# Optimization experiments

Hardware: AMD Instinct MI355X
Metric: run time of the kernel (lower is better)

## Reference

```python
import jax, jax.numpy as jnp
import numpy as np
from jax import lax

TAU = 10.0
THR = 1.0
ALPHA = float(np.exp(-1.0 / TAU))  # leak factor exp(-dt/tau), dt=1


def conv2d(x, w, pad):
    # x: [N,C,H,W], w: [O,I,kh,kw]
    return lax.conv_general_dilated(
        x, w, window_strides=(1, 1), padding=[(pad, pad), (pad, pad)],
        dimension_numbers=('NCHW', 'OIHW', 'NCHW'))


def avgpool(x, k):
    n, c, h, w = x.shape
    return x.reshape(n, c, h // k, k, w // k, k).mean(axis=(3, 5))


def exp_leak(x):
    # x: [T, ...]; v[t] = alpha*v[t-1] + x[t]; outputs membrane each step
    def step(v, xt):
        v = ALPHA * v + xt
        return v, v
    _, y = lax.scan(step, jnp.zeros_like(x[0]), x)
    return y


def lif(x):
    # LIF with SingleSpike + MembraneSubtract reset (norm_input=False)
    def step(v, xt):
        v = ALPHA * v + xt
        s = (v >= THR).astype(v.dtype)
        return v - s * THR, s
    _, s = lax.scan(step, jnp.zeros_like(x[0]), x)
    return s


def forward(x, conv1_w, conv2_w, lin_w):
    B, T = x.shape[:2]
    h = avgpool(conv2d(x.reshape(B * T, 2, 32, 32), conv1_w, 2), 4)  # [BT,4,8,8]
    h = h.reshape(B, T, 4, 8, 8).swapaxes(0, 1)                       # [T,B,4,8,8]
    h = lif(exp_leak(h)).swapaxes(0, 1).reshape(B * T, 4, 8, 8)
    h = avgpool(conv2d(h, conv2_w, 1), 2)                             # [BT,8,4,4]
    h = h.reshape(B, T, 8, 4, 4).swapaxes(0, 1)                       # [T,B,8,4,4]
    h = lif(exp_leak(h)).swapaxes(0, 1).reshape(B, T, 8 * 4 * 4)      # [B,T,128]
    return jnp.einsum('btf,of->bto', h, lin_w)                        # [B,T,2]


def setup_inputs() -> dict:
    key = jax.random.key(0)
    k1, k2, k3, k4 = jax.random.split(key, 4)
    B, T = 128, 100
    x = jax.random.uniform(k1, (B, T, 2, 32, 32), dtype=jnp.float32)
    conv1_w = jax.random.normal(k2, (4, 2, 5, 5), dtype=jnp.float32) / np.sqrt(2 * 5 * 5)
    conv2_w = jax.random.normal(k3, (8, 4, 3, 3), dtype=jnp.float32) / np.sqrt(4 * 3 * 3)
    lin_w = jax.random.normal(k4, (2, 128), dtype=jnp.float32) / np.sqrt(128)
    return {'x': x, 'conv1_w': conv1_w, 'conv2_w': conv2_w, 'lin_w': lin_w}


def reference(x, conv1_w, conv2_w, lin_w):
    return forward(x, conv1_w, conv2_w, lin_w)
```

## Files before the change

kernel.cpp:

```cpp
#include <hip/hip_runtime.h>

#define ALPHA 0.90483741803595957f

__global__ void prep_weights(const float* __restrict__ w1, const float* __restrict__ w2,
                             float* __restrict__ w1e, float* __restrict__ w2e) {
    int idx = blockIdx.x * 256 + threadIdx.x;
    if (idx < 512) {
        int v = idx & 7, u = (idx >> 3) & 7, ch = (idx >> 6) & 1, oc = idx >> 7;
        float s = 0.f;
        for (int a = 0; a < 5; ++a) {
            int i = u - a; if (i < 0 || i > 3) continue;
            for (int b = 0; b < 5; ++b) {
                int j = v - b; if (j < 0 || j > 3) continue;
                s += w1[((oc * 2 + ch) * 5 + a) * 5 + b];
            }
        }
        w1e[idx] = s * (1.f / 16.f);
    } else if (idx < 1024) {
        int k = idx - 512;
        int v = k & 3, u = (k >> 2) & 3, ch = (k >> 4) & 3, oc = k >> 6;
        float s = 0.f;
        for (int a = 0; a < 3; ++a) {
            int i = u - a; if (i < 0 || i > 1) continue;
            for (int b = 0; b < 3; ++b) {
                int j = v - b; if (j < 0 || j > 1) continue;
                s += w2[((oc * 4 + ch) * 3 + a) * 3 + b];
            }
        }
        w2e[k] = s * 0.25f;
    }
}

__global__ __launch_bounds__(256) void conv1_pool(const float* __restrict__ x,
                                                  const float* __restrict__ w1e,
                                                  float* __restrict__ y1) {
    __shared__ __align__(16) float tile[4][2][36][36];
    int tid = threadIdx.x;

    float4* t4 = (float4*)&tile[0][0][0][0];
    #pragma unroll
    for (int k = 0; k < 11; ++k) {
        int i = tid + k * 256;
        if (i < 2592) t4[i] = make_float4(0.f, 0.f, 0.f, 0.f);
    }
    __syncthreads();

    int li = tid >> 6, pos = tid & 63;
    long gi = (long)blockIdx.x * 4 + li;
    const float* src = x + gi * 2048;
    #pragma unroll
    for (int k = 0; k < 8; ++k) {
        int e = k * 256 + pos * 4;
        float4 d = *(const float4*)(src + e);
        int ch = e >> 10, rem = e & 1023, r = rem >> 5, c = rem & 31;
        float* dst = &tile[li][ch][r + 2][c + 2];
        dst[0] = d.x; dst[1] = d.y; dst[2] = d.z; dst[3] = d.w;
    }
    __syncthreads();

    int p = pos >> 3, q = pos & 7;
    float acc0 = 0.f, acc1 = 0.f, acc2 = 0.f, acc3 = 0.f;
    #pragma unroll
    for (int ch = 0; ch < 2; ++ch) {
        #pragma unroll
        for (int r = 0; r < 8; ++r) {
            const float* row = &tile[li][ch][4 * p + r][4 * q];
            float4 a = *(const float4*)row;
            float4 b = *(const float4*)(row + 4);
            float in[8] = {a.x, a.y, a.z, a.w, b.x, b.y, b.z, b.w};
            #pragma unroll
            for (int c = 0; c < 8; ++c) {
                float xi = in[c];
                acc0 += w1e[((0 * 2 + ch) * 8 + r) * 8 + c] * xi;
                acc1 += w1e[((1 * 2 + ch) * 8 + r) * 8 + c] * xi;
                acc2 += w1e[((2 * 2 + ch) * 8 + r) * 8 + c] * xi;
                acc3 += w1e[((3 * 2 + ch) * 8 + r) * 8 + c] * xi;
            }
        }
    }
    float* dst = y1 + gi * 256 + pos;
    dst[0] = acc0; dst[64] = acc1; dst[128] = acc2; dst[192] = acc3;
}

__global__ __launch_bounds__(256) void fused_tail(const float* __restrict__ y1,
                                                  const float* __restrict__ w2e,
                                                  const float* __restrict__ lw,
                                                  float* __restrict__ out) {
    __shared__ float tile[4][10][10];
    __shared__ float red[2][2];
    int tid = threadIdx.x;
    int b = blockIdx.x;

    for (int i = tid; i < 400; i += 256) ((float*)tile)[i] = 0.f;

    int ch1 = tid >> 6, r1 = (tid >> 3) & 7, c1 = tid & 7;
    float* tslot = &tile[ch1][r1 + 1][c1 + 1];

    int oc = tid >> 4, p = (tid >> 2) & 3, q = tid & 3;
    float wts[64];
    float lw0 = 0.f, lw1 = 0.f;
    if (tid < 128) {
        #pragma unroll
        for (int k = 0; k < 64; ++k) wts[k] = w2e[oc * 64 + k];
        lw0 = lw[tid];
        lw1 = lw[128 + tid];
    }
    const float* base = &tile[0][2 * p][2 * q];

    const float* src = y1 + (long)b * 100 * 256 + tid;
    float* outp = out + (long)b * 200;

    float cur = src[0];
    float nxt = src[256];
    float v1 = 0.f, v2 = 0.f, v1b = 0.f, v2b = 0.f;

    __syncthreads();

    for (int t = 0; t < 100; ++t) {
        float nn = (t + 2 < 100) ? src[(t + 2) * 256] : 0.f;

        v1 = ALPHA * v1 + cur;
        v2 = ALPHA * v2 + v1;
        float s = (v2 >= 1.f) ? 1.f : 0.f;
        v2 -= s;
        *tslot = s;
        __syncthreads();

        if (tid < 128) {
            float acc = 0.f;
            #pragma unroll
            for (int ch = 0; ch < 4; ++ch) {
                #pragma unroll
                for (int r = 0; r < 4; ++r) {
                    const float* row = base + ch * 100 + r * 10;
                    float2 u = *(const float2*)row;
                    float2 w = *(const float2*)(row + 2);
                    acc += wts[ch * 16 + r * 4 + 0] * u.x;
                    acc += wts[ch * 16 + r * 4 + 1] * u.y;
                    acc += wts[ch * 16 + r * 4 + 2] * w.x;
                    acc += wts[ch * 16 + r * 4 + 3] * w.y;
                }
            }
            v1b = ALPHA * v1b + acc;
            v2b = ALPHA * v2b + v1b;
            float s2 = (v2b >= 1.f) ? 1.f : 0.f;
            v2b -= s2;

            float a0 = s2 * lw0;
            float a1 = s2 * lw1;
            #pragma unroll
            for (int off = 32; off; off >>= 1) {
                a0 += __shfl_xor(a0, off);
                a1 += __shfl_xor(a1, off);
            }
            if ((tid & 63) == 0) { red[tid >> 6][0] = a0; red[tid >> 6][1] = a1; }
        }
        __syncthreads();
        if (tid == 0) {
            float2 o2;
            o2.x = red[0][0] + red[1][0];
            o2.y = red[0][1] + red[1][1];
            *(float2*)(outp + t * 2) = o2;
        }
        cur = nxt; nxt = nn;
    }
}

extern "C" void kernel_launch(void* const* d_in, const int* in_sizes, int n_in,
                              void* d_out, int out_size, void* d_ws, size_t ws_size,
                              hipStream_t stream) {
    const float* x  = (const float*)d_in[0];
    const float* w1 = (const float*)d_in[1];
    const float* w2 = (const float*)d_in[2];
    const float* lw = (const float*)d_in[3];
    float* out = (float*)d_out;

    float* ws   = (float*)d_ws;
    float* w1e  = ws;
    float* w2e  = ws + 512;
    float* y1   = ws + 1024;

    prep_weights<<<4, 256, 0, stream>>>(w1, w2, w1e, w2e);
    conv1_pool<<<3200, 256, 0, stream>>>(x, w1e, y1);
    fused_tail<<<128, 256, 0, stream>>>(y1, w2e, lw, out);
}
```

Before: 250.0 us.

## Collapse sequential tail to single-wavefront blocks and split out linear layer

The 256-thread sequential LIF tail becomes a 64-lane single-wavefront kernel. Each lane handles four first-layer neurons and two conv2 output channels, with spike tiles stored channel-interleaved for float4 LDS reads. The per-step cross-wave reduction and the final linear projection move into a separate fully parallel kernel that reads second-layer spikes from workspace. This targets block-level barrier and reduction cost in the 100-step serial loop, at the price of extra global traffic, an extra launch, and only 128 wavefronts of parallelism for the serial part.

```diff
diff --git a/kernel.cpp b/kernel.cpp
--- a/kernel.cpp
+++ b/kernel.cpp
@@ -82,88 +82,119 @@
     dst[0] = acc0; dst[64] = acc1; dst[128] = acc2; dst[192] = acc3;
 }
 
-__global__ __launch_bounds__(256) void fused_tail(const float* __restrict__ y1,
-                                                  const float* __restrict__ w2e,
+__global__ __launch_bounds__(64, 1) void fused_wave(const float* __restrict__ y1,
+                                                    const float* __restrict__ w2e,
+                                                    float* __restrict__ s2g) {
+    __shared__ float tile[808];
+    int lane = threadIdx.x;
+    int b = blockIdx.x;
+
+    #pragma unroll
+    for (int k = 0; k < 13; ++k) {
+        int i = lane + k * 64;
+        if (i < 808) tile[i] = 0.f;
+    }
+
+    int r1 = lane >> 3, c1 = lane & 7;
+    int posq = (r1 + 1) * 10 + (c1 + 1);
+    float* wrA = &tile[posq * 4];
+    float* wrB = &tile[404 + posq * 4];
+
+    int oc = lane >> 4, p = (lane >> 2) & 3, q = lane & 3;
+
+    float wa[64], wb[64];
+    #pragma unroll
+    for (int k = 0; k < 16; ++k) {
+        float4 ta = *(const float4*)(w2e + oc * 64 + k * 4);
+        float4 tb = *(const float4*)(w2e + (oc + 4) * 64 + k * 4);
+        wa[k * 4 + 0] = ta.x; wa[k * 4 + 1] = ta.y; wa[k * 4 + 2] = ta.z; wa[k * 4 + 3] = ta.w;
+        wb[k * 4 + 0] = tb.x; wb[k * 4 + 1] = tb.y; wb[k * 4 + 2] = tb.z; wb[k * 4 + 3] = tb.w;
+    }
+
+    const float* rbase = &tile[((2 * p) * 10 + 2 * q) * 4];
+    if (p & 1) rbase += 404;
+
+    const float* src = y1 + (long)b * 25600 + lane;
+    float* dst = s2g + (long)b * 100 * 128 + lane;
+
+    float cur0 = src[0], cur1 = src[64], cur2 = src[128], cur3 = src[192];
+    float v10 = 0.f, v20 = 0.f, v11 = 0.f, v21 = 0.f;
+    float v12 = 0.f, v22 = 0.f, v13 = 0.f, v23 = 0.f;
+    float w1a = 0.f, w2a = 0.f, w1b = 0.f, w2b = 0.f;
+
+    __syncthreads();
+
+    for (int t = 0; t < 100; ++t) {
+        const float* nsrc = src + (t < 99 ? (t + 1) * 256 : 0);
+        float n0 = nsrc[0], n1 = nsrc[64], n2 = nsrc[128], n3 = nsrc[192];
+
+        v10 = ALPHA * v10 + cur0; v20 = ALPHA * v20 + v10;
+        float s0 = (v20 >= 1.f) ? 1.f : 0.f; v20 -= s0;
+        v11 = ALPHA * v11 + cur1; v21 = ALPHA * v21 + v11;
+        float s1 = (v21 >= 1.f) ? 1.f : 0.f; v21 -= s1;
+        v12 = ALPHA * v12 + cur2; v22 = ALPHA * v22 + v12;
+        float s2 = (v22 >= 1.f) ? 1.f : 0.f; v22 -= s2;
+        v13 = ALPHA * v13 + cur3; v23 = ALPHA * v23 + v13;
+        float s3 = (v23 >= 1.f) ? 1.f : 0.f; v23 -= s3;
+
+        float4 sp = make_float4(s0, s1, s2, s3);
+        *(float4*)wrA = sp;
+        *(float4*)wrB = sp;
+        __syncthreads();
+
+        float qv[64];
+        #pragma unroll
+        for (int rr = 0; rr < 4; ++rr) {
+            #pragma unroll
+            for (int cc = 0; cc < 4; ++cc) {
+                float4 tq = *(const float4*)(rbase + rr * 40 + cc * 4);
+                int o = (rr * 4 + cc) * 4;
+                qv[o + 0] = tq.x; qv[o + 1] = tq.y; qv[o + 2] = tq.z; qv[o + 3] = tq.w;
+            }
+        }
+
+        float acca = 0.f, accb = 0.f;
+        #pragma unroll
+        for (int ch = 0; ch < 4; ++ch)
+            #pragma unroll
+            for (int rr = 0; rr < 4; ++rr)
+                #pragma unroll
+                for (int cc = 0; cc < 4; ++cc) {
+                    float xv = qv[(rr * 4 + cc) * 4 + ch];
+                    acca += wa[ch * 16 + rr * 4 + cc] * xv;
+                    accb += wb[ch * 16 + rr * 4 + cc] * xv;
+                }
+
+        w1a = ALPHA * w1a + acca; w2a = ALPHA * w2a + w1a;
+        float sa = (w2a >= 1.f) ? 1.f : 0.f; w2a -= sa;
+        w1b = ALPHA * w1b + accb; w2b = ALPHA * w2b + w1b;
+        float sb = (w2b >= 1.f) ? 1.f : 0.f; w2b -= sb;
+
+        dst[t * 128] = sa;
+        dst[t * 128 + 64] = sb;
+
+        __syncthreads();
+        cur0 = n0; cur1 = n1; cur2 = n2; cur3 = n3;
+    }
+}
+
+__global__ __launch_bounds__(256) void linear_out(const float* __restrict__ s2,
                                                   const float* __restrict__ lw,
                                                   float* __restrict__ out) {
-    __shared__ float tile[4][10][10];
-    __shared__ float red[2][2];
     int tid = threadIdx.x;
-    int b = blockIdx.x;
-
-    for (int i = tid; i < 400; i += 256) ((float*)tile)[i] = 0.f;
-
-    int ch1 = tid >> 6, r1 = (tid >> 3) & 7, c1 = tid & 7;
-    float* tslot = &tile[ch1][r1 + 1][c1 + 1];
-
-    int oc = tid >> 4, p = (tid >> 2) & 3, q = tid & 3;
-    float wts[64];
-    float lw0 = 0.f, lw1 = 0.f;
-    if (tid < 128) {
-        #pragma unroll
-        for (int k = 0; k < 64; ++k) wts[k] = w2e[oc * 64 + k];
-        lw0 = lw[tid];
-        lw1 = lw[128 + tid];
-    }
-    const float* base = &tile[0][2 * p][2 * q];
-
-    const float* src = y1 + (long)b * 100 * 256 + tid;
-    float* outp = out + (long)b * 200;
-
-    float cur = src[0];
-    float nxt = src[256];
-    float v1 = 0.f, v2 = 0.f, v1b = 0.f, v2b = 0.f;
-
-    __syncthreads();
-
-    for (int t = 0; t < 100; ++t) {
-        float nn = (t + 2 < 100) ? src[(t + 2) * 256] : 0.f;
-
-        v1 = ALPHA * v1 + cur;
-        v2 = ALPHA * v2 + v1;
-        float s = (v2 >= 1.f) ? 1.f : 0.f;
-        v2 -= s;
-        *tslot = s;
-        __syncthreads();
-
-        if (tid < 128) {
-            float acc = 0.f;
-            #pragma unroll
-            for (int ch = 0; ch < 4; ++ch) {
-                #pragma unroll
-                for (int r = 0; r < 4; ++r) {
-                    const float* row = base + ch * 100 + r * 10;
-                    float2 u = *(const float2*)row;
-                    float2 w = *(const float2*)(row + 2);
-                    acc += wts[ch * 16 + r * 4 + 0] * u.x;
-                    acc += wts[ch * 16 + r * 4 + 1] * u.y;
-                    acc += wts[ch * 16 + r * 4 + 2] * w.x;
-                    acc += wts[ch * 16 + r * 4 + 3] * w.y;
-                }
-            }
-            v1b = ALPHA * v1b + acc;
-            v2b = ALPHA * v2b + v1b;
-            float s2 = (v2b >= 1.f) ? 1.f : 0.f;
-            v2b -= s2;
-
-            float a0 = s2 * lw0;
-            float a1 = s2 * lw1;
-            #pragma unroll
-            for (int off = 32; off; off >>= 1) {
-                a0 += __shfl_xor(a0, off);
-                a1 += __shfl_xor(a1, off);
-            }
-            if ((tid & 63) == 0) { red[tid >> 6][0] = a0; red[tid >> 6][1] = a1; }
-        }
-        __syncthreads();
-        if (tid == 0) {
-            float2 o2;
-            o2.x = red[0][0] + red[1][0];
-            o2.y = red[0][1] + red[1][1];
-            *(float2*)(outp + t * 2) = o2;
-        }
-        cur = nxt; nxt = nn;
-    }
+    long bt = (long)blockIdx.x * 4 + (tid >> 6);
+    int lane = tid & 63;
+    float2 v = *(const float2*)(s2 + bt * 128 + lane * 2);
+    float w00 = lw[lane * 2], w01 = lw[lane * 2 + 1];
+    float w10 = lw[128 + lane * 2], w11 = lw[128 + lane * 2 + 1];
+    float a0 = v.x * w00 + v.y * w01;
+    float a1 = v.x * w10 + v.y * w11;
+    #pragma unroll
+    for (int off = 32; off; off >>= 1) {
+        a0 += __shfl_down(a0, off);
+        a1 += __shfl_down(a1, off);
+    }
+    if (lane == 0) { out[bt * 2] = a0; out[bt * 2 + 1] = a1; }
 }
 
 extern "C" void kernel_launch(void* const* d_in, const int* in_sizes, int n_in,
@@ -179,8 +210,10 @@
     float* w1e  = ws;
     float* w2e  = ws + 512;
     float* y1   = ws + 1024;
+    float* s2g  = y1 + 3276800;
 
     prep_weights<<<4, 256, 0, stream>>>(w1, w2, w1e, w2e);
     conv1_pool<<<3200, 256, 0, stream>>>(x, w1e, y1);
-    fused_tail<<<128, 256, 0, stream>>>(y1, w2e, lw, out);
-}
+    fused_wave<<<128, 64, 0, stream>>>(y1, w2e, s2g);
+    linear_out<<<3200, 256, 0, stream>>>(s2g, lw, out);
+}
```

After: 215.9 us. -13.6%, faster.
